# Performance work log

Measured on AMD Instinct MI355X. Metric: run time of the kernel, lower is better.

The kernel has to match this reference:

```python
import jax, jax.numpy as jnp
import numpy as np
import math

K = 2
CAPACITY = -1
NEED_L_AUX = True


def topk_gating(logits, k=K, capacity=CAPACITY, need_l_aux=NEED_L_AUX):
    # logits: (T, P, E) tokens x prototypes x experts-per-prototype
    gates = jax.nn.softmax(logits.astype(jnp.float32), axis=-1).astype(logits.dtype)
    T, P, E = gates.shape
    cap = int(math.ceil(1.25 * T / E)) if capacity < 0 else capacity

    idx1 = jnp.argmax(gates, axis=-1)                      # (T, P)
    mask1 = jax.nn.one_hot(idx1, E, dtype=jnp.int32)       # (T, P, E)
    loc1 = jnp.cumsum(mask1, axis=0) - 1                   # position in expert queue
    if need_l_aux:
        me = jnp.mean(gates, axis=0)
        ce = jnp.mean(mask1.astype(jnp.float32), axis=0)
        l_aux = jnp.mean(me * ce)
    else:
        l_aux = jnp.zeros((), jnp.float32)
    mask1 = mask1 * (loc1 < cap)                           # drop over-capacity tokens
    loc1_s = jnp.sum(loc1 * mask1, axis=-1)                # (T, P)
    gates1_s = jnp.sum(gates * mask1, axis=-1)
    denom = gates1_s
    gates_s_list = [gates1_s]
    mask_list = [mask1]
    loc_s_list = [loc1_s]
    last_logits = logits
    last_mask = mask1
    prev_masks = mask1
    for _ in range(2, k + 1):
        last_logits = jnp.where(last_mask.astype(bool), -jnp.inf, last_logits)
        idx = jnp.argmax(last_logits, axis=-1)
        mask = jax.nn.one_hot(idx, E, dtype=jnp.int32)
        loc = jnp.cumsum(mask, axis=0) - 1 + jnp.sum(prev_masks, axis=0, keepdims=True)
        mask = mask * (loc < cap)
        last_mask = mask
        prev_masks = prev_masks + mask
        mask_list.append(mask)
        loc_s_list.append(jnp.sum(loc * mask, axis=-1))
        gs = jnp.sum(gates * mask, axis=-1)
        denom = denom + gs
        gates_s_list.append(gs)
    denom = jnp.maximum(denom, jnp.finfo(denom.dtype).eps)

    combine = jnp.zeros((T, P, E, cap), gates.dtype)
    for gs, mask, ls in zip(gates_s_list, mask_list, loc_s_list):
        g = (gs / denom)[..., None] * mask                  # (T, P, E)
        loc_sc = jax.nn.one_hot(ls, cap, dtype=gates.dtype)  # (T, P, cap)
        combine = combine + g[..., None] * loc_sc[:, :, None, :]
    dispatch_mask = combine.astype(bool)
    return l_aux.astype(logits.dtype), combine.astype(logits.dtype), dispatch_mask


def setup_inputs() -> dict:
    key = jax.random.key(0)
    k1, k2 = jax.random.split(key)
    inp = jax.random.normal(k1, (4096, 2048), dtype=jnp.float32)
    W = jax.random.normal(k2, (64, 2048), dtype=jnp.float32) / math.sqrt(2048.0)
    return {"input": inp, "W": W, "bs": 4096, "prototypes": 2}


def reference(input, W, bs, prototypes):
    logits = input @ W.T                                   # (T, num_experts_total)
    logits = logits.reshape(input.shape[0], prototypes, -1)  # (T, P, E)
    return topk_gating(logits, k=K, capacity=CAPACITY, need_l_aux=NEED_L_AUX)
```

## Files before the change

kernel.cpp:

```cpp
#include <hip/hip_runtime.h>
#include <cstdint>

#define T_TOK 4096
#define KDIM 2048
#define NE 64
#define NP 2
#define EE 32
#define CAP 160
#define NKC 8
#define KCHUNK 256
#define BLKR 128
#define COMB_ELEMS 41943040ull
#define OUT_ELEMS 83886081ull
#define SMALLF 65536
#define NFB 4096
#define TOT4 20971520

__global__ __launch_bounds__(256) void k_fused(const float* __restrict__ x,
                                               const float* __restrict__ W,
                                               float* __restrict__ part,
                                               float* __restrict__ out,
                                               int s1lo, int s1hi, int s2lo, int s2hi,
                                               int fillLast) {
  __shared__ float xs[BLKR][36];
  __shared__ float wt[32][68];
  const int tid = threadIdx.x;
  if (blockIdx.x >= 256) {
    const int fb = blockIdx.x - 256;
    float4* p4 = reinterpret_cast<float4*>(out);
    const float4 z4 = make_float4(0.f, 0.f, 0.f, 0.f);
    const int start = fb * 5120;
#pragma unroll
    for (int j = 0; j < 20; ++j) {
      const int i4 = start + tid + j * 256;
      if (i4 >= s1lo && i4 < s1hi) continue;
      if (i4 >= s2lo && i4 < s2hi) continue;
      p4[i4] = z4;
    }
    if (fillLast && fb == NFB - 1 && tid == 255) out[OUT_ELEMS - 1] = 0.f;
    return;
  }
  const int rb = blockIdx.x & 31;
  const int kc = blockIdx.x >> 5;
  const int r0 = rb * BLKR;
  const int er = tid & 15;
  const int rg = tid >> 4;
  float acc[8][4];
#pragma unroll
  for (int i = 0; i < 8; ++i)
#pragma unroll
    for (int c = 0; c < 4; ++c) acc[i][c] = 0.f;

  float4 sx[4], sw[2];
  {
    const int kb = kc * KCHUNK;
#pragma unroll
    for (int q = 0; q < 4; ++q) {
      const int li = tid + q * 256, row = li >> 3, kq = (li & 7) * 4;
      sx[q] = *reinterpret_cast<const float4*>(&x[(size_t)(r0 + row) * KDIM + kb + kq]);
    }
#pragma unroll
    for (int q = 0; q < 2; ++q) {
      const int li = tid + q * 256, e = li >> 3, kq = (li & 7) * 4;
      sw[q] = *reinterpret_cast<const float4*>(&W[(size_t)e * KDIM + kb + kq]);
    }
  }
  for (int s = 0; s < 8; ++s) {
    __syncthreads();
#pragma unroll
    for (int q = 0; q < 4; ++q) {
      const int li = tid + q * 256, row = li >> 3, kq = (li & 7) * 4;
      *reinterpret_cast<float4*>(&xs[row][kq]) = sx[q];
    }
#pragma unroll
    for (int q = 0; q < 2; ++q) {
      const int li = tid + q * 256, e = li >> 3, kq = (li & 7) * 4;
      wt[kq][e] = sw[q].x; wt[kq + 1][e] = sw[q].y;
      wt[kq + 2][e] = sw[q].z; wt[kq + 3][e] = sw[q].w;
    }
    if (s < 7) {
      const int kb = kc * KCHUNK + (s + 1) * 32;
#pragma unroll
      for (int q = 0; q < 4; ++q) {
        const int li = tid + q * 256, row = li >> 3, kq = (li & 7) * 4;
        sx[q] = *reinterpret_cast<const float4*>(&x[(size_t)(r0 + row) * KDIM + kb + kq]);
      }
#pragma unroll
      for (int q = 0; q < 2; ++q) {
        const int li = tid + q * 256, e = li >> 3, kq = (li & 7) * 4;
        sw[q] = *reinterpret_cast<const float4*>(&W[(size_t)e * KDIM + kb + kq]);
      }
    }
    __syncthreads();
#pragma unroll
    for (int k4 = 0; k4 < 8; ++k4) {
      float4 wb[4];
#pragma unroll
      for (int j = 0; j < 4; ++j)
        wb[j] = *reinterpret_cast<const float4*>(&wt[k4 * 4 + j][er * 4]);
#pragma unroll
      for (int i = 0; i < 8; ++i) {
        const float4 xv = *reinterpret_cast<const float4*>(&xs[rg + 16 * i][k4 * 4]);
        acc[i][0] = fmaf(xv.w, wb[3].x, fmaf(xv.z, wb[2].x, fmaf(xv.y, wb[1].x, fmaf(xv.x, wb[0].x, acc[i][0]))));
        acc[i][1] = fmaf(xv.w, wb[3].y, fmaf(xv.z, wb[2].y, fmaf(xv.y, wb[1].y, fmaf(xv.x, wb[0].y, acc[i][1]))));
        acc[i][2] = fmaf(xv.w, wb[3].z, fmaf(xv.z, wb[2].z, fmaf(xv.y, wb[1].z, fmaf(xv.x, wb[0].z, acc[i][2]))));
        acc[i][3] = fmaf(xv.w, wb[3].w, fmaf(xv.z, wb[2].w, fmaf(xv.y, wb[1].w, fmaf(xv.x, wb[0].w, acc[i][3]))));
      }
    }
  }
#pragma unroll
  for (int i = 0; i < 8; ++i) {
    float4 v; v.x = acc[i][0]; v.y = acc[i][1]; v.z = acc[i][2]; v.w = acc[i][3];
    *reinterpret_cast<float4*>(
        &part[((size_t)kc * T_TOK + r0 + rg + 16 * i) * NE + er * 4]) = v;
  }
}

__global__ __launch_bounds__(256) void k_fill2(float* __restrict__ out) {
  float4* p4 = reinterpret_cast<float4*>(out + 4);
  const float4 z4 = make_float4(0.f, 0.f, 0.f, 0.f);
  const int base = blockIdx.x * 2048 + threadIdx.x;
#pragma unroll
  for (int j = 0; j < 8; ++j) p4[base + j * 256] = z4;
}

__global__ __launch_bounds__(64) void k_soft(const float* __restrict__ part,
                                             float2* __restrict__ g12,
                                             int* __restrict__ idxs,
                                             float* __restrict__ me_part) {
  __shared__ float lg[64][33];
  const int tid = threadIdx.x;
  const int R = blockIdx.x * 64 + tid;
  const int t = R >> 1;
  const int p = R & 1;
  float v[32];
  const float* pr = part + (size_t)t * NE + p * EE;
#pragma unroll
  for (int e = 0; e < 32; e += 4) {
    float4 s = *reinterpret_cast<const float4*>(pr + e);
    v[e] = s.x; v[e + 1] = s.y; v[e + 2] = s.z; v[e + 3] = s.w;
  }
  for (int kc = 1; kc < NKC; ++kc) {
    const float* prk = pr + (size_t)kc * T_TOK * NE;
#pragma unroll
    for (int e = 0; e < 32; e += 4) {
      float4 s = *reinterpret_cast<const float4*>(prk + e);
      v[e] += s.x; v[e + 1] += s.y; v[e + 2] += s.z; v[e + 3] += s.w;
    }
  }
  float m = v[0];
#pragma unroll
  for (int e = 1; e < 32; ++e) m = fmaxf(m, v[e]);
  float sum = 0.f;
#pragma unroll
  for (int e = 0; e < 32; ++e) { v[e] = expf(v[e] - m); sum += v[e]; }
  const float inv = 1.0f / sum;
#pragma unroll
  for (int e = 0; e < 32; ++e) v[e] *= inv;
  float g1 = -1.f; int i1 = 0;
#pragma unroll
  for (int e = 0; e < 32; ++e) if (v[e] > g1) { g1 = v[e]; i1 = e; }
  float g2 = -1.f; int i2 = 0;
#pragma unroll
  for (int e = 0; e < 32; ++e) if (e != i1 && v[e] > g2) { g2 = v[e]; i2 = e; }
  g12[R] = make_float2(g1, g2);
  idxs[R] = i1 | (i2 << 8);
#pragma unroll
  for (int e = 0; e < 32; ++e) lg[tid][e] = v[e];
  __syncthreads();
  {
    const int pp = tid >> 5, ee = tid & 31;
    float s = 0.f;
    for (int rr = pp; rr < 64; rr += 2) s += lg[rr][ee];
    me_part[blockIdx.x * 64 + tid] = s;
  }
}

__global__ __launch_bounds__(1024) void k_scan(const int* __restrict__ idxs,
                                               const float2* __restrict__ g12,
                                               const float* __restrict__ me_part,
                                               int2* __restrict__ fl,
                                               float2* __restrict__ wvp,
                                               float* __restrict__ out) {
  __shared__ int grp[NP][64][32];
  __shared__ int tot[NP][32];
  __shared__ unsigned short tk1[NP][T_TOK];
  __shared__ unsigned short tk2[NP][T_TOK];
  __shared__ float red[64];
  const int tid = threadIdx.x;
  const int wvi = tid >> 6;
  const int p = wvi >> 3;
  const int wg = wvi & 7;
  const int l = tid & 63;
  const unsigned long long lmask = (1ull << l) - 1ull;
  for (int gi = 0; gi < 8; ++gi) {
    const int g = wg * 8 + gi;
    const int t = g * 64 + l;
    const int e1 = idxs[t * 2 + p] & 255;
    if (l < 32) grp[p][g][l] = 0;
    unsigned long long m = ~0ull;
#pragma unroll
    for (int b = 0; b < 5; ++b) {
      const unsigned long long bm = __ballot((e1 >> b) & 1);
      m &= ((e1 >> b) & 1) ? bm : ~bm;
    }
    const int rank = (int)__popcll(m & lmask);
    if (rank == 0) grp[p][g][e1] = (int)__popcll(m);
    tk1[p][t] = (unsigned short)(rank | (e1 << 6));
  }
  __syncthreads();
  if (tid < 64) {
    const int pp = tid >> 5, ee = tid & 31;
    int s = 0;
    for (int g = 0; g < 64; ++g) { int vv = grp[pp][g][ee]; grp[pp][g][ee] = s; s += vv; }
    tot[pp][ee] = s;
  }
  __syncthreads();
  for (int gi = 0; gi < 8; ++gi) {
    const int g = wg * 8 + gi;
    const int t = g * 64 + l;
    const int vv = tk1[p][t];
    tk1[p][t] = (unsigned short)(grp[p][g][vv >> 6] + (vv & 63));
  }
  if (tid < 64) {
    float s = 0.f;
    for (int b = 0; b < 128; ++b) s += me_part[b * 64 + tid];
    red[tid] = s * (float)tot[tid >> 5][tid & 31];
  }
  __syncthreads();
  if (tid == 0) {
    float s = 0.f;
    for (int i = 0; i < 64; ++i) s += red[i];
    out[0] = s / (64.0f * 4096.0f * 4096.0f);
  }
  for (int gi = 0; gi < 8; ++gi) {
    const int g = wg * 8 + gi;
    const int t = g * 64 + l;
    const int ii = idxs[t * 2 + p];
    const int e2 = (tk1[p][t] < CAP) ? (ii >> 8) : (ii & 255);
    if (l < 32) grp[p][g][l] = 0;
    unsigned long long m = ~0ull;
#pragma unroll
    for (int b = 0; b < 5; ++b) {
      const unsigned long long bm = __ballot((e2 >> b) & 1);
      m &= ((e2 >> b) & 1) ? bm : ~bm;
    }
    const int rank = (int)__popcll(m & lmask);
    if (rank == 0) grp[p][g][e2] = (int)__popcll(m);
    tk2[p][t] = (unsigned short)(rank | (e2 << 6));
  }
  __syncthreads();
  if (tid < 64) {
    const int pp = tid >> 5, ee = tid & 31;
    int s = min(tot[pp][ee], CAP);
    for (int g = 0; g < 64; ++g) { int vv = grp[pp][g][ee]; grp[pp][g][ee] = s; s += vv; }
  }
  __syncthreads();
  for (int gi = 0; gi < 8; ++gi) {
    const int g = wg * 8 + gi;
    const int t = g * 64 + l;
    const int R = t * 2 + p;
    const int ii = idxs[R];
    const int e1 = ii & 255;
    const int loc1v = tk1[p][t];
    const bool kept1 = loc1v < CAP;
    const int v2 = tk2[p][t];
    const int rank2 = v2 & 63, e2 = v2 >> 6;
    const int loc2 = grp[p][g][e2] + rank2;
    const bool kept2 = loc2 < CAP;
    const float2 gg = g12[R];
    const float gs1 = kept1 ? gg.x : 0.f;
    const float g2v = kept1 ? gg.y : gg.x;
    const float gs2 = kept2 ? g2v : 0.f;
    const float den = fmaxf(gs1 + gs2, 1.1920929e-07f);
    fl[R] = make_int2(kept1 ? e1 * CAP + loc1v : -1, kept2 ? e2 * CAP + loc2 : -1);
    wvp[R] = make_float2(gs1 / den, gs2 / den);
  }
}

__global__ __launch_bounds__(256) void k_fix(const int2* __restrict__ fl,
                                             const float2* __restrict__ wvp,
                                             float* __restrict__ out,
                                             int rlimit) {
  const int R = blockIdx.x * 256 + threadIdx.x;
  const int2 f = fl[R];
  const float2 w = wvp[R];
  float* oc = out + 1 + (size_t)R * 5120;
  if (f.x >= 0) oc[f.x] = w.x;
  if (f.y >= 0) oc[f.y] = w.y;
  if (R < rlimit) {
    float* od = out + 1 + COMB_ELEMS + (size_t)R * 5120;
    if (f.x >= 0) od[f.x] = 1.0f;
    if (f.y >= 0) od[f.y] = 1.0f;
  }
}

__global__ __launch_bounds__(1024) void k_write_tail(const int2* __restrict__ fl,
                                                     float* __restrict__ out,
                                                     int nfullB) {
  __shared__ int2 sfl[16];
  const int tid = threadIdx.x;
  const int rstart = nfullB * 2;
  const int nr = 8192 - rstart;
  if (tid < nr) sfl[tid] = fl[rstart + tid];
  __syncthreads();
  const size_t base = 1 + COMB_ELEMS + (size_t)rstart * 5120;
  const int cnt = nr * 5120;
  const int nx4 = (cnt - 4) >> 2;
  float4* p4 = (float4*)(out + base + 3);
  const float4 z4 = make_float4(0.f, 0.f, 0.f, 0.f);
  for (int idx = tid; idx < nx4; idx += 1024) p4[idx] = z4;
  if (tid < 3) out[base + tid] = 0.f;
  if (tid == 3) out[base + cnt - 1] = 0.f;
  __syncthreads();
  if (tid < 2 * nr) {
    const int rr = rstart + (tid >> 1);
    const int2 f = sfl[tid >> 1];
    const int pos = (tid & 1) ? f.y : f.x;
    if (pos >= 0) out[1 + COMB_ELEMS + (size_t)rr * 5120 + pos] = 1.0f;
  }
}

extern "C" void kernel_launch(void* const* d_in, const int* in_sizes, int n_in,
                              void* d_out, int out_size, void* d_ws, size_t ws_size,
                              hipStream_t stream) {
  const float* x = (const float*)d_in[0];
  const float* W = (const float*)d_in[1];
  float* out = (float*)d_out;

  const size_t PARTF = (size_t)NKC * T_TOK * NE;

  float* small;
  float* part;
  int s1lo = 0, s1hi = 0, s2lo = 0, s2hi = 0, fillLast = 1;
  bool needFill2 = false;
  int nfullB = 4096, rlimit = 8192;
  if (ws_size >= (SMALLF + PARTF) * sizeof(float)) {
    small = (float*)d_ws;
    part = small + SMALLF;
  } else if (ws_size >= SMALLF * sizeof(float)) {
    small = (float*)d_ws;
    part = out + 4;
    s1lo = 1; s1hi = 1 + (int)(PARTF / 4);
    needFill2 = true;
  } else {
    const size_t tb = (OUT_ELEMS - SMALLF) & ~(size_t)3;
    small = out + tb;
    part = out + 4;
    s1lo = 1; s1hi = 1 + (int)(PARTF / 4);
    s2lo = (int)(tb / 4); s2hi = TOT4;
    fillLast = 0;
    needFill2 = true;
    nfullB = (int)((tb - 1 - COMB_ELEMS) / 10240);
    rlimit = nfullB * 2;
  }
  float2* g12 = (float2*)small;
  int* idxs = (int*)(small + 16384);
  float* me_part = small + 24576;
  int2* fl = (int2*)(small + 32768);
  float2* wvp = (float2*)(small + 49152);

  hipLaunchKernelGGL(k_fused, dim3(256 + NFB), dim3(256), 0, stream,
                     x, W, part, out, s1lo, s1hi, s2lo, s2hi, fillLast);
  hipLaunchKernelGGL(k_soft, dim3(128), dim3(64), 0, stream, part, g12, idxs, me_part);
  if (needFill2)
    hipLaunchKernelGGL(k_fill2, dim3(256), dim3(256), 0, stream, out);
  hipLaunchKernelGGL(k_scan, dim3(1), dim3(1024), 0, stream, idxs, g12, me_part, fl, wvp, out);
  hipLaunchKernelGGL(k_fix, dim3(32), dim3(256), 0, stream, fl, wvp, out, rlimit);
  if (nfullB < 4096)
    hipLaunchKernelGGL(k_write_tail, dim3(1), dim3(1024), 0, stream, fl, out, nfullB);
}
```

Baseline: 104.0 us.

## Fuse softmax/top-2 into GEMM blocks, dropping split-K partials

```diff
diff --git a/kernel.cpp b/kernel.cpp
--- a/kernel.cpp
+++ b/kernel.cpp
@@ -7,89 +7,65 @@
 #define NP 2
 #define EE 32
 #define CAP 160
-#define NKC 8
-#define KCHUNK 256
-#define BLKR 128
 #define COMB_ELEMS 41943040ull
 #define OUT_ELEMS 83886081ull
 #define SMALLF 65536
 #define NFB 4096
+#define NGB 128
 #define TOT4 20971520
 
 __global__ __launch_bounds__(256) void k_fused(const float* __restrict__ x,
                                                const float* __restrict__ W,
-                                               float* __restrict__ part,
+                                               float2* __restrict__ g12,
+                                               int* __restrict__ idxs,
+                                               float* __restrict__ me_part,
                                                float* __restrict__ out,
-                                               int s1lo, int s1hi, int s2lo, int s2hi,
-                                               int fillLast) {
-  __shared__ float xs[BLKR][36];
+                                               int s2lo, int s2hi, int fillLast) {
+  __shared__ float xs[32][36];
   __shared__ float wt[32][68];
   const int tid = threadIdx.x;
-  if (blockIdx.x >= 256) {
-    const int fb = blockIdx.x - 256;
+  if (blockIdx.x >= NGB) {
+    const int fb = blockIdx.x - NGB;
     float4* p4 = reinterpret_cast<float4*>(out);
     const float4 z4 = make_float4(0.f, 0.f, 0.f, 0.f);
     const int start = fb * 5120;
 #pragma unroll
     for (int j = 0; j < 20; ++j) {
       const int i4 = start + tid + j * 256;
-      if (i4 >= s1lo && i4 < s1hi) continue;
       if (i4 >= s2lo && i4 < s2hi) continue;
       p4[i4] = z4;
     }
     if (fillLast && fb == NFB - 1 && tid == 255) out[OUT_ELEMS - 1] = 0.f;
     return;
   }
-  const int rb = blockIdx.x & 31;
-  const int kc = blockIdx.x >> 5;
-  const int r0 = rb * BLKR;
+  const int r0 = blockIdx.x * 32;
   const int er = tid & 15;
   const int rg = tid >> 4;
-  float acc[8][4];
-#pragma unroll
-  for (int i = 0; i < 8; ++i)
-#pragma unroll
-    for (int c = 0; c < 4; ++c) acc[i][c] = 0.f;
-
-  float4 sx[4], sw[2];
+  const int lrow = tid >> 3, lkq = (tid & 7) * 4;
+  float tot[2][4], chunk[2][4];
+#pragma unroll
+  for (int i = 0; i < 2; ++i)
+#pragma unroll
+    for (int c = 0; c < 4; ++c) chunk[i][c] = 0.f;
+
+  float4 sx, sw0, sw1;
   {
-    const int kb = kc * KCHUNK;
-#pragma unroll
-    for (int q = 0; q < 4; ++q) {
-      const int li = tid + q * 256, row = li >> 3, kq = (li & 7) * 4;
-      sx[q] = *reinterpret_cast<const float4*>(&x[(size_t)(r0 + row) * KDIM + kb + kq]);
-    }
-#pragma unroll
-    for (int q = 0; q < 2; ++q) {
-      const int li = tid + q * 256, e = li >> 3, kq = (li & 7) * 4;
-      sw[q] = *reinterpret_cast<const float4*>(&W[(size_t)e * KDIM + kb + kq]);
-    }
-  }
-  for (int s = 0; s < 8; ++s) {
+    sx = *reinterpret_cast<const float4*>(&x[(size_t)(r0 + lrow) * KDIM + lkq]);
+    sw0 = *reinterpret_cast<const float4*>(&W[(size_t)lrow * KDIM + lkq]);
+    sw1 = *reinterpret_cast<const float4*>(&W[(size_t)(lrow + 32) * KDIM + lkq]);
+  }
+  for (int it = 0; it < 64; ++it) {
     __syncthreads();
-#pragma unroll
-    for (int q = 0; q < 4; ++q) {
-      const int li = tid + q * 256, row = li >> 3, kq = (li & 7) * 4;
-      *reinterpret_cast<float4*>(&xs[row][kq]) = sx[q];
-    }
-#pragma unroll
-    for (int q = 0; q < 2; ++q) {
-      const int li = tid + q * 256, e = li >> 3, kq = (li & 7) * 4;
-      wt[kq][e] = sw[q].x; wt[kq + 1][e] = sw[q].y;
-      wt[kq + 2][e] = sw[q].z; wt[kq + 3][e] = sw[q].w;
-    }
-    if (s < 7) {
-      const int kb = kc * KCHUNK + (s + 1) * 32;
-#pragma unroll
-      for (int q = 0; q < 4; ++q) {
-        const int li = tid + q * 256, row = li >> 3, kq = (li & 7) * 4;
-        sx[q] = *reinterpret_cast<const float4*>(&x[(size_t)(r0 + row) * KDIM + kb + kq]);
-      }
-#pragma unroll
-      for (int q = 0; q < 2; ++q) {
-        const int li = tid + q * 256, e = li >> 3, kq = (li & 7) * 4;
-        sw[q] = *reinterpret_cast<const float4*>(&W[(size_t)e * KDIM + kb + kq]);
-      }
+    *reinterpret_cast<float4*>(&xs[lrow][lkq]) = sx;
+    wt[lkq][lrow] = sw0.x; wt[lkq + 1][lrow] = sw0.y;
+    wt[lkq + 2][lrow] = sw0.z; wt[lkq + 3][lrow] = sw0.w;
+    wt[lkq][lrow + 32] = sw1.x; wt[lkq + 1][lrow + 32] = sw1.y;
+    wt[lkq + 2][lrow + 32] = sw1.z; wt[lkq + 3][lrow + 32] = sw1.w;
+    if (it < 63) {
+      const int kb = (it + 1) * 32;
+      sx = *reinterpret_cast<const float4*>(&x[(size_t)(r0 + lrow) * KDIM + kb + lkq]);
+      sw0 = *reinterpret_cast<const float4*>(&W[(size_t)lrow * KDIM + kb + lkq]);
+      sw1 = *reinterpret_cast<const float4*>(&W[(size_t)(lrow + 32) * KDIM + kb + lkq]);
     }
     __syncthreads();
 #pragma unroll
@@ -99,79 +75,69 @@
       for (int j = 0; j < 4; ++j)
         wb[j] = *reinterpret_cast<const float4*>(&wt[k4 * 4 + j][er * 4]);
 #pragma unroll
-      for (int i = 0; i < 8; ++i) {
-        const float4 xv = *reinterpret_cast<const float4*>(&xs[rg + 16 * i][k4 * 4]);
-        acc[i][0] = fmaf(xv.w, wb[3].x, fmaf(xv.z, wb[2].x, fmaf(xv.y, wb[1].x, fmaf(xv.x, wb[0].x, acc[i][0]))));
-        acc[i][1] = fmaf(xv.w, wb[3].y, fmaf(xv.z, wb[2].y, fmaf(xv.y, wb[1].y, fmaf(xv.x, wb[0].y, acc[i][1]))));
-        acc[i][2] = fmaf(xv.w, wb[3].z, fmaf(xv.z, wb[2].z, fmaf(xv.y, wb[1].z, fmaf(xv.x, wb[0].z, acc[i][2]))));
-        acc[i][3] = fmaf(xv.w, wb[3].w, fmaf(xv.z, wb[2].w, fmaf(xv.y, wb[1].w, fmaf(xv.x, wb[0].w, acc[i][3]))));
+      for (int i = 0; i < 2; ++i) {
+        const float4 xv = *reinterpret_cast<const float4*>(&xs[rg * 2 + i][k4 * 4]);
+        chunk[i][0] = fmaf(xv.w, wb[3].x, fmaf(xv.z, wb[2].x, fmaf(xv.y, wb[1].x, fmaf(xv.x, wb[0].x, chunk[i][0]))));
+        chunk[i][1] = fmaf(xv.w, wb[3].y, fmaf(xv.z, wb[2].y, fmaf(xv.y, wb[1].y, fmaf(xv.x, wb[0].y, chunk[i][1]))));
+        chunk[i][2] = fmaf(xv.w, wb[3].z, fmaf(xv.z, wb[2].z, fmaf(xv.y, wb[1].z, fmaf(xv.x, wb[0].z, chunk[i][2]))));
+        chunk[i][3] = fmaf(xv.w, wb[3].w, fmaf(xv.z, wb[2].w, fmaf(xv.y, wb[1].w, fmaf(xv.x, wb[0].w, chunk[i][3]))));
       }
     }
-  }
-#pragma unroll
-  for (int i = 0; i < 8; ++i) {
-    float4 v; v.x = acc[i][0]; v.y = acc[i][1]; v.z = acc[i][2]; v.w = acc[i][3];
-    *reinterpret_cast<float4*>(
-        &part[((size_t)kc * T_TOK + r0 + rg + 16 * i) * NE + er * 4]) = v;
-  }
-}
-
-__global__ __launch_bounds__(256) void k_fill2(float* __restrict__ out) {
-  float4* p4 = reinterpret_cast<float4*>(out + 4);
-  const float4 z4 = make_float4(0.f, 0.f, 0.f, 0.f);
-  const int base = blockIdx.x * 2048 + threadIdx.x;
-#pragma unroll
-  for (int j = 0; j < 8; ++j) p4[base + j * 256] = z4;
-}
-
-__global__ __launch_bounds__(64) void k_soft(const float* __restrict__ part,
-                                             float2* __restrict__ g12,
-                                             int* __restrict__ idxs,
-                                             float* __restrict__ me_part) {
-  __shared__ float lg[64][33];
-  const int tid = threadIdx.x;
-  const int R = blockIdx.x * 64 + tid;
-  const int t = R >> 1;
-  const int p = R & 1;
-  float v[32];
-  const float* pr = part + (size_t)t * NE + p * EE;
-#pragma unroll
-  for (int e = 0; e < 32; e += 4) {
-    float4 s = *reinterpret_cast<const float4*>(pr + e);
-    v[e] = s.x; v[e + 1] = s.y; v[e + 2] = s.z; v[e + 3] = s.w;
-  }
-  for (int kc = 1; kc < NKC; ++kc) {
-    const float* prk = pr + (size_t)kc * T_TOK * NE;
+    if ((it & 7) == 7) {
+#pragma unroll
+      for (int i = 0; i < 2; ++i)
+#pragma unroll
+        for (int c = 0; c < 4; ++c) {
+          if (it == 7) tot[i][c] = chunk[i][c];
+          else tot[i][c] += chunk[i][c];
+          chunk[i][c] = 0.f;
+        }
+    }
+  }
+  __syncthreads();
+#pragma unroll
+  for (int i = 0; i < 2; ++i) {
+    float4 v; v.x = tot[i][0]; v.y = tot[i][1]; v.z = tot[i][2]; v.w = tot[i][3];
+    *reinterpret_cast<float4*>(&wt[rg * 2 + i][er * 4]) = v;
+  }
+  __syncthreads();
+  if (tid < 64) {
+    const int row = tid >> 1, p = tid & 1;
+    float v[32];
 #pragma unroll
     for (int e = 0; e < 32; e += 4) {
-      float4 s = *reinterpret_cast<const float4*>(prk + e);
-      v[e] += s.x; v[e + 1] += s.y; v[e + 2] += s.z; v[e + 3] += s.w;
-    }
-  }
-  float m = v[0];
-#pragma unroll
-  for (int e = 1; e < 32; ++e) m = fmaxf(m, v[e]);
-  float sum = 0.f;
-#pragma unroll
-  for (int e = 0; e < 32; ++e) { v[e] = expf(v[e] - m); sum += v[e]; }
-  const float inv = 1.0f / sum;
-#pragma unroll
-  for (int e = 0; e < 32; ++e) v[e] *= inv;
-  float g1 = -1.f; int i1 = 0;
-#pragma unroll
-  for (int e = 0; e < 32; ++e) if (v[e] > g1) { g1 = v[e]; i1 = e; }
-  float g2 = -1.f; int i2 = 0;
-#pragma unroll
-  for (int e = 0; e < 32; ++e) if (e != i1 && v[e] > g2) { g2 = v[e]; i2 = e; }
-  g12[R] = make_float2(g1, g2);
-  idxs[R] = i1 | (i2 << 8);
-#pragma unroll
-  for (int e = 0; e < 32; ++e) lg[tid][e] = v[e];
-  __syncthreads();
-  {
+      const float4 s = *reinterpret_cast<const float4*>(&wt[row][p * 32 + e]);
+      v[e] = s.x; v[e + 1] = s.y; v[e + 2] = s.z; v[e + 3] = s.w;
+    }
+    float m = v[0];
+#pragma unroll
+    for (int e = 1; e < 32; ++e) m = fmaxf(m, v[e]);
+    float sum = 0.f;
+#pragma unroll
+    for (int e = 0; e < 32; ++e) { v[e] = expf(v[e] - m); sum += v[e]; }
+    const float inv = 1.0f / sum;
+#pragma unroll
+    for (int e = 0; e < 32; ++e) v[e] *= inv;
+    float g1 = -1.f; int i1 = 0;
+#pragma unroll
+    for (int e = 0; e < 32; ++e) if (v[e] > g1) { g1 = v[e]; i1 = e; }
+    float g2 = -1.f; int i2 = 0;
+#pragma unroll
+    for (int e = 0; e < 32; ++e) if (e != i1 && v[e] > g2) { g2 = v[e]; i2 = e; }
+    const int R = blockIdx.x * 64 + tid;
+    g12[R] = make_float2(g1, g2);
+    idxs[R] = i1 | (i2 << 8);
+#pragma unroll
+    for (int e = 0; e < 32; e += 4) {
+      float4 s; s.x = v[e]; s.y = v[e + 1]; s.z = v[e + 2]; s.w = v[e + 3];
+      *reinterpret_cast<float4*>(&wt[row][p * 32 + e]) = s;
+    }
+  }
+  __syncthreads();
+  if (tid < 64) {
     const int pp = tid >> 5, ee = tid & 31;
     float s = 0.f;
-    for (int rr = pp; rr < 64; rr += 2) s += lg[rr][ee];
+    for (int tok = 0; tok < 32; ++tok) s += wt[tok][pp * 32 + ee];
     me_part[blockIdx.x * 64 + tid] = s;
   }
 }
@@ -328,29 +294,16 @@
   const float* W = (const float*)d_in[1];
   float* out = (float*)d_out;
 
-  const size_t PARTF = (size_t)NKC * T_TOK * NE;
-
   float* small;
-  float* part;
-  int s1lo = 0, s1hi = 0, s2lo = 0, s2hi = 0, fillLast = 1;
-  bool needFill2 = false;
+  int s2lo = 0, s2hi = 0, fillLast = 1;
   int nfullB = 4096, rlimit = 8192;
-  if (ws_size >= (SMALLF + PARTF) * sizeof(float)) {
+  if (ws_size >= SMALLF * sizeof(float)) {
     small = (float*)d_ws;
-    part = small + SMALLF;
-  } else if (ws_size >= SMALLF * sizeof(float)) {
-    small = (float*)d_ws;
-    part = out + 4;
-    s1lo = 1; s1hi = 1 + (int)(PARTF / 4);
-    needFill2 = true;
   } else {
     const size_t tb = (OUT_ELEMS - SMALLF) & ~(size_t)3;
     small = out + tb;
-    part = out + 4;
-    s1lo = 1; s1hi = 1 + (int)(PARTF / 4);
     s2lo = (int)(tb / 4); s2hi = TOT4;
     fillLast = 0;
-    needFill2 = true;
     nfullB = (int)((tb - 1 - COMB_ELEMS) / 10240);
     rlimit = nfullB * 2;
   }
@@ -360,11 +313,8 @@
   int2* fl = (int2*)(small + 32768);
   float2* wvp = (float2*)(small + 49152);
 
-  hipLaunchKernelGGL(k_fused, dim3(256 + NFB), dim3(256), 0, stream,
-                     x, W, part, out, s1lo, s1hi, s2lo, s2hi, fillLast);
-  hipLaunchKernelGGL(k_soft, dim3(128), dim3(64), 0, stream, part, g12, idxs, me_part);
-  if (needFill2)
-    hipLaunchKernelGGL(k_fill2, dim3(256), dim3(256), 0, stream, out);
+  hipLaunchKernelGGL(k_fused, dim3(NGB + NFB), dim3(256), 0, stream,
+                     x, W, g12, idxs, me_part, out, s2lo, s2hi, fillLast);
   hipLaunchKernelGGL(k_scan, dim3(1), dim3(1024), 0, stream, idxs, g12, me_part, fl, wvp, out);
   hipLaunchKernelGGL(k_fix, dim3(32), dim3(256), 0, stream, fl, wvp, out, rlimit);
   if (nfullB < 4096)
```

New measurement: 125.9 us. +21.1%, slower.

## Fuse GEMM, softmax and output zero-fill into one cooperative persistent kernel

Applied to the files above, without the earlier changes.

```diff
diff --git a/kernel.cpp b/kernel.cpp
--- a/kernel.cpp
+++ b/kernel.cpp
@@ -1,5 +1,8 @@
 #include <hip/hip_runtime.h>
+#include <hip/hip_cooperative_groups.h>
 #include <cstdint>
+
+namespace cg = cooperative_groups;
 
 #define T_TOK 4096
 #define KDIM 2048
@@ -12,74 +15,61 @@
 #define BLKR 128
 #define COMB_ELEMS 41943040ull
 #define OUT_ELEMS 83886081ull
-#define SMALLF 65536
+#define SMALLF 65544
+#define PARTF 2097152ull
+#define TOT4 20971520
 #define NFB 4096
-#define TOT4 20971520
-
-__global__ __launch_bounds__(256) void k_fused(const float* __restrict__ x,
-                                               const float* __restrict__ W,
-                                               float* __restrict__ part,
-                                               float* __restrict__ out,
-                                               int s1lo, int s1hi, int s2lo, int s2hi,
-                                               int fillLast) {
-  __shared__ float xs[BLKR][36];
-  __shared__ float wt[32][68];
+#define UNITS 16384u
+#define RESERVE_B 1024u
+#define PB_F 81788928
+
+__device__ __forceinline__ void fill_units(float* __restrict__ out,
+                                           unsigned int* __restrict__ ctr,
+                                           unsigned int ubase, unsigned int uend,
+                                           int lane, int s1lo, int s1hi) {
+  float4* p4 = reinterpret_cast<float4*>(out);
+  const float4 z4 = make_float4(0.f, 0.f, 0.f, 0.f);
+  while (true) {
+    unsigned int u = 0;
+    if (lane == 0) u = atomicAdd(ctr, 1u);
+    u = (unsigned int)__builtin_amdgcn_readfirstlane((int)u) + ubase;
+    if (u >= uend) break;
+    const int b4 = (int)u * 1280 + lane;
+#pragma unroll
+    for (int j = 0; j < 20; ++j) {
+      const int i4 = b4 + j * 64;
+      if (i4 >= s1lo && i4 < s1hi) continue;
+      p4[i4] = z4;
+    }
+  }
+}
+
+__global__ __launch_bounds__(256)
+void k_coop(const float* __restrict__ x, const float* __restrict__ W,
+            float* __restrict__ part, float2* __restrict__ g12,
+            int* __restrict__ idxs, float* __restrict__ me_part,
+            float* __restrict__ out, unsigned int* __restrict__ ctr,
+            int s1lo, int s1hi) {
+  __shared__ union {
+    struct { float xs[BLKR][36]; float wt[32][68]; } g;
+    float lg[64][33];
+  } sh;
   const int tid = threadIdx.x;
-  if (blockIdx.x >= 256) {
-    const int fb = blockIdx.x - 256;
-    float4* p4 = reinterpret_cast<float4*>(out);
-    const float4 z4 = make_float4(0.f, 0.f, 0.f, 0.f);
-    const int start = fb * 5120;
-#pragma unroll
-    for (int j = 0; j < 20; ++j) {
-      const int i4 = start + tid + j * 256;
-      if (i4 >= s1lo && i4 < s1hi) continue;
-      if (i4 >= s2lo && i4 < s2hi) continue;
-      p4[i4] = z4;
-    }
-    if (fillLast && fb == NFB - 1 && tid == 255) out[OUT_ELEMS - 1] = 0.f;
-    return;
-  }
-  const int rb = blockIdx.x & 31;
-  const int kc = blockIdx.x >> 5;
-  const int r0 = rb * BLKR;
-  const int er = tid & 15;
-  const int rg = tid >> 4;
-  float acc[8][4];
-#pragma unroll
-  for (int i = 0; i < 8; ++i)
-#pragma unroll
-    for (int c = 0; c < 4; ++c) acc[i][c] = 0.f;
-
-  float4 sx[4], sw[2];
-  {
-    const int kb = kc * KCHUNK;
-#pragma unroll
-    for (int q = 0; q < 4; ++q) {
-      const int li = tid + q * 256, row = li >> 3, kq = (li & 7) * 4;
-      sx[q] = *reinterpret_cast<const float4*>(&x[(size_t)(r0 + row) * KDIM + kb + kq]);
-    }
-#pragma unroll
-    for (int q = 0; q < 2; ++q) {
-      const int li = tid + q * 256, e = li >> 3, kq = (li & 7) * 4;
-      sw[q] = *reinterpret_cast<const float4*>(&W[(size_t)e * KDIM + kb + kq]);
-    }
-  }
-  for (int s = 0; s < 8; ++s) {
-    __syncthreads();
-#pragma unroll
-    for (int q = 0; q < 4; ++q) {
-      const int li = tid + q * 256, row = li >> 3, kq = (li & 7) * 4;
-      *reinterpret_cast<float4*>(&xs[row][kq]) = sx[q];
-    }
-#pragma unroll
-    for (int q = 0; q < 2; ++q) {
-      const int li = tid + q * 256, e = li >> 3, kq = (li & 7) * 4;
-      wt[kq][e] = sw[q].x; wt[kq + 1][e] = sw[q].y;
-      wt[kq + 2][e] = sw[q].z; wt[kq + 3][e] = sw[q].w;
-    }
-    if (s < 7) {
-      const int kb = kc * KCHUNK + (s + 1) * 32;
+  const int lane = tid & 63;
+  if (blockIdx.x < 256) {
+    const int rb = (int)blockIdx.x & 31;
+    const int kc = (int)blockIdx.x >> 5;
+    const int r0 = rb * BLKR;
+    const int er = tid & 15;
+    const int rg = tid >> 4;
+    float acc[8][4];
+#pragma unroll
+    for (int i = 0; i < 8; ++i)
+#pragma unroll
+      for (int c = 0; c < 4; ++c) acc[i][c] = 0.f;
+    float4 sx[4], sw[2];
+    {
+      const int kb = kc * KCHUNK;
 #pragma unroll
       for (int q = 0; q < 4; ++q) {
         const int li = tid + q * 256, row = li >> 3, kq = (li & 7) * 4;
@@ -91,89 +81,109 @@
         sw[q] = *reinterpret_cast<const float4*>(&W[(size_t)e * KDIM + kb + kq]);
       }
     }
+    for (int s = 0; s < 8; ++s) {
+      __syncthreads();
+#pragma unroll
+      for (int q = 0; q < 4; ++q) {
+        const int li = tid + q * 256, row = li >> 3, kq = (li & 7) * 4;
+        *reinterpret_cast<float4*>(&sh.g.xs[row][kq]) = sx[q];
+      }
+#pragma unroll
+      for (int q = 0; q < 2; ++q) {
+        const int li = tid + q * 256, e = li >> 3, kq = (li & 7) * 4;
+        sh.g.wt[kq][e] = sw[q].x; sh.g.wt[kq + 1][e] = sw[q].y;
+        sh.g.wt[kq + 2][e] = sw[q].z; sh.g.wt[kq + 3][e] = sw[q].w;
+      }
+      if (s < 7) {
+        const int kb = kc * KCHUNK + (s + 1) * 32;
+#pragma unroll
+        for (int q = 0; q < 4; ++q) {
+          const int li = tid + q * 256, row = li >> 3, kq = (li & 7) * 4;
+          sx[q] = *reinterpret_cast<const float4*>(&x[(size_t)(r0 + row) * KDIM + kb + kq]);
+        }
+#pragma unroll
+        for (int q = 0; q < 2; ++q) {
+          const int li = tid + q * 256, e = li >> 3, kq = (li & 7) * 4;
+          sw[q] = *reinterpret_cast<const float4*>(&W[(size_t)e * KDIM + kb + kq]);
+        }
+      }
+      __syncthreads();
+#pragma unroll
+      for (int k4 = 0; k4 < 8; ++k4) {
+        float4 wb[4];
+#pragma unroll
+        for (int j = 0; j < 4; ++j)
+          wb[j] = *reinterpret_cast<const float4*>(&sh.g.wt[k4 * 4 + j][er * 4]);
+#pragma unroll
+        for (int i = 0; i < 8; ++i) {
+          const float4 xv = *reinterpret_cast<const float4*>(&sh.g.xs[rg + 16 * i][k4 * 4]);
+          acc[i][0] = fmaf(xv.w, wb[3].x, fmaf(xv.z, wb[2].x, fmaf(xv.y, wb[1].x, fmaf(xv.x, wb[0].x, acc[i][0]))));
+          acc[i][1] = fmaf(xv.w, wb[3].y, fmaf(xv.z, wb[2].y, fmaf(xv.y, wb[1].y, fmaf(xv.x, wb[0].y, acc[i][1]))));
+          acc[i][2] = fmaf(xv.w, wb[3].z, fmaf(xv.z, wb[2].z, fmaf(xv.y, wb[1].z, fmaf(xv.x, wb[0].z, acc[i][2]))));
+          acc[i][3] = fmaf(xv.w, wb[3].w, fmaf(xv.z, wb[2].w, fmaf(xv.y, wb[1].w, fmaf(xv.x, wb[0].w, acc[i][3]))));
+        }
+      }
+    }
+#pragma unroll
+    for (int i = 0; i < 8; ++i) {
+      float4 v; v.x = acc[i][0]; v.y = acc[i][1]; v.z = acc[i][2]; v.w = acc[i][3];
+      *reinterpret_cast<float4*>(
+          &part[((size_t)kc * T_TOK + r0 + rg + 16 * i) * NE + er * 4]) = v;
+    }
+  }
+  fill_units(out, ctr, 0u, UNITS - RESERVE_B, lane, s1lo, s1hi);
+  __threadfence();
+  cg::this_grid().sync();
+  if (blockIdx.x < 128) {
+    const int un = (int)blockIdx.x;
+    if (tid < 64) {
+      const int R = un * 64 + tid;
+      const int t = R >> 1, p = R & 1;
+      float v[32];
+      const float* pr = part + (size_t)t * NE + p * EE;
+#pragma unroll
+      for (int e = 0; e < 32; e += 4) {
+        const float4 s = *reinterpret_cast<const float4*>(pr + e);
+        v[e] = s.x; v[e + 1] = s.y; v[e + 2] = s.z; v[e + 3] = s.w;
+      }
+      for (int kc = 1; kc < NKC; ++kc) {
+        const float* prk = pr + (size_t)kc * T_TOK * NE;
+#pragma unroll
+        for (int e = 0; e < 32; e += 4) {
+          const float4 s = *reinterpret_cast<const float4*>(prk + e);
+          v[e] += s.x; v[e + 1] += s.y; v[e + 2] += s.z; v[e + 3] += s.w;
+        }
+      }
+      float m = v[0];
+#pragma unroll
+      for (int e = 1; e < 32; ++e) m = fmaxf(m, v[e]);
+      float sum = 0.f;
+#pragma unroll
+      for (int e = 0; e < 32; ++e) { v[e] = expf(v[e] - m); sum += v[e]; }
+      const float inv = 1.0f / sum;
+#pragma unroll
+      for (int e = 0; e < 32; ++e) v[e] *= inv;
+      float g1 = -1.f; int i1 = 0;
+#pragma unroll
+      for (int e = 0; e < 32; ++e) if (v[e] > g1) { g1 = v[e]; i1 = e; }
+      float g2 = -1.f; int i2 = 0;
+#pragma unroll
+      for (int e = 0; e < 32; ++e) if (e != i1 && v[e] > g2) { g2 = v[e]; i2 = e; }
+      g12[R] = make_float2(g1, g2);
+      idxs[R] = i1 | (i2 << 8);
+#pragma unroll
+      for (int e = 0; e < 32; ++e) sh.lg[tid][e] = v[e];
+    }
     __syncthreads();
-#pragma unroll
-    for (int k4 = 0; k4 < 8; ++k4) {
-      float4 wb[4];
-#pragma unroll
-      for (int j = 0; j < 4; ++j)
-        wb[j] = *reinterpret_cast<const float4*>(&wt[k4 * 4 + j][er * 4]);
-#pragma unroll
-      for (int i = 0; i < 8; ++i) {
-        const float4 xv = *reinterpret_cast<const float4*>(&xs[rg + 16 * i][k4 * 4]);
-        acc[i][0] = fmaf(xv.w, wb[3].x, fmaf(xv.z, wb[2].x, fmaf(xv.y, wb[1].x, fmaf(xv.x, wb[0].x, acc[i][0]))));
-        acc[i][1] = fmaf(xv.w, wb[3].y, fmaf(xv.z, wb[2].y, fmaf(xv.y, wb[1].y, fmaf(xv.x, wb[0].y, acc[i][1]))));
-        acc[i][2] = fmaf(xv.w, wb[3].z, fmaf(xv.z, wb[2].z, fmaf(xv.y, wb[1].z, fmaf(xv.x, wb[0].z, acc[i][2]))));
-        acc[i][3] = fmaf(xv.w, wb[3].w, fmaf(xv.z, wb[2].w, fmaf(xv.y, wb[1].w, fmaf(xv.x, wb[0].w, acc[i][3]))));
-      }
-    }
-  }
-#pragma unroll
-  for (int i = 0; i < 8; ++i) {
-    float4 v; v.x = acc[i][0]; v.y = acc[i][1]; v.z = acc[i][2]; v.w = acc[i][3];
-    *reinterpret_cast<float4*>(
-        &part[((size_t)kc * T_TOK + r0 + rg + 16 * i) * NE + er * 4]) = v;
-  }
-}
-
-__global__ __launch_bounds__(256) void k_fill2(float* __restrict__ out) {
-  float4* p4 = reinterpret_cast<float4*>(out + 4);
-  const float4 z4 = make_float4(0.f, 0.f, 0.f, 0.f);
-  const int base = blockIdx.x * 2048 + threadIdx.x;
-#pragma unroll
-  for (int j = 0; j < 8; ++j) p4[base + j * 256] = z4;
-}
-
-__global__ __launch_bounds__(64) void k_soft(const float* __restrict__ part,
-                                             float2* __restrict__ g12,
-                                             int* __restrict__ idxs,
-                                             float* __restrict__ me_part) {
-  __shared__ float lg[64][33];
-  const int tid = threadIdx.x;
-  const int R = blockIdx.x * 64 + tid;
-  const int t = R >> 1;
-  const int p = R & 1;
-  float v[32];
-  const float* pr = part + (size_t)t * NE + p * EE;
-#pragma unroll
-  for (int e = 0; e < 32; e += 4) {
-    float4 s = *reinterpret_cast<const float4*>(pr + e);
-    v[e] = s.x; v[e + 1] = s.y; v[e + 2] = s.z; v[e + 3] = s.w;
-  }
-  for (int kc = 1; kc < NKC; ++kc) {
-    const float* prk = pr + (size_t)kc * T_TOK * NE;
-#pragma unroll
-    for (int e = 0; e < 32; e += 4) {
-      float4 s = *reinterpret_cast<const float4*>(prk + e);
-      v[e] += s.x; v[e + 1] += s.y; v[e + 2] += s.z; v[e + 3] += s.w;
-    }
-  }
-  float m = v[0];
-#pragma unroll
-  for (int e = 1; e < 32; ++e) m = fmaxf(m, v[e]);
-  float sum = 0.f;
-#pragma unroll
-  for (int e = 0; e < 32; ++e) { v[e] = expf(v[e] - m); sum += v[e]; }
-  const float inv = 1.0f / sum;
-#pragma unroll
-  for (int e = 0; e < 32; ++e) v[e] *= inv;
-  float g1 = -1.f; int i1 = 0;
-#pragma unroll
-  for (int e = 0; e < 32; ++e) if (v[e] > g1) { g1 = v[e]; i1 = e; }
-  float g2 = -1.f; int i2 = 0;
-#pragma unroll
-  for (int e = 0; e < 32; ++e) if (e != i1 && v[e] > g2) { g2 = v[e]; i2 = e; }
-  g12[R] = make_float2(g1, g2);
-  idxs[R] = i1 | (i2 << 8);
-#pragma unroll
-  for (int e = 0; e < 32; ++e) lg[tid][e] = v[e];
-  __syncthreads();
-  {
-    const int pp = tid >> 5, ee = tid & 31;
-    float s = 0.f;
-    for (int rr = pp; rr < 64; rr += 2) s += lg[rr][ee];
-    me_part[blockIdx.x * 64 + tid] = s;
-  }
+    if (tid < 64) {
+      const int pp = tid >> 5, ee = tid & 31;
+      float s = 0.f;
+      for (int rr = pp; rr < 64; rr += 2) s += sh.lg[rr][ee];
+      me_part[un * 64 + tid] = s;
+    }
+    __syncthreads();
+  }
+  fill_units(out, ctr + 1, UNITS - RESERVE_B, UNITS, lane, s1lo, s1hi);
 }
 
 __global__ __launch_bounds__(1024) void k_scan(const int* __restrict__ idxs,
@@ -278,10 +288,191 @@
   }
 }
 
-__global__ __launch_bounds__(256) void k_fix(const int2* __restrict__ fl,
-                                             const float2* __restrict__ wvp,
-                                             float* __restrict__ out,
-                                             int rlimit) {
+__global__ __launch_bounds__(256) void k_fix2(const int2* __restrict__ fl,
+                                              const float2* __restrict__ wvp,
+                                              float* __restrict__ out) {
+  const int R = blockIdx.x * 256 + threadIdx.x;
+  const int2 f = fl[R];
+  const float2 w = wvp[R];
+  float* oc = out + 1 + (size_t)R * 5120;
+  float* od = out + 1 + COMB_ELEMS + (size_t)R * 5120;
+  if (R == 8191) od[5119] = 0.f;
+  if (f.x >= 0) { oc[f.x] = w.x; od[f.x] = 1.0f; }
+  if (f.y >= 0) { oc[f.y] = w.y; od[f.y] = 1.0f; }
+}
+
+__global__ __launch_bounds__(256) void k_tailB(float* __restrict__ out) {
+  float4* p4 = reinterpret_cast<float4*>(out);
+  const float4 z4 = make_float4(0.f, 0.f, 0.f, 0.f);
+  const int base = 20447232 + (int)blockIdx.x * 4096 + (int)threadIdx.x;
+#pragma unroll
+  for (int j = 0; j < 16; ++j) p4[base + j * 256] = z4;
+  if (blockIdx.x == 0 && threadIdx.x == 0) out[OUT_ELEMS - 1] = 0.f;
+}
+
+__global__ __launch_bounds__(256) void k_fusedF(const float* __restrict__ x,
+                                                const float* __restrict__ W,
+                                                float* __restrict__ part,
+                                                float* __restrict__ out,
+                                                int s1lo, int s1hi, int s2lo, int s2hi,
+                                                int fillLast) {
+  __shared__ float xs[BLKR][36];
+  __shared__ float wt[32][68];
+  const int tid = threadIdx.x;
+  if (blockIdx.x >= 256) {
+    const int fb = blockIdx.x - 256;
+    float4* p4 = reinterpret_cast<float4*>(out);
+    const float4 z4 = make_float4(0.f, 0.f, 0.f, 0.f);
+    const int start = fb * 5120;
+#pragma unroll
+    for (int j = 0; j < 20; ++j) {
+      const int i4 = start + tid + j * 256;
+      if (i4 >= s1lo && i4 < s1hi) continue;
+      if (i4 >= s2lo && i4 < s2hi) continue;
+      p4[i4] = z4;
+    }
+    if (fillLast && fb == NFB - 1 && tid == 255) out[OUT_ELEMS - 1] = 0.f;
+    return;
+  }
+  const int rb = blockIdx.x & 31;
+  const int kc = blockIdx.x >> 5;
+  const int r0 = rb * BLKR;
+  const int er = tid & 15;
+  const int rg = tid >> 4;
+  float acc[8][4];
+#pragma unroll
+  for (int i = 0; i < 8; ++i)
+#pragma unroll
+    for (int c = 0; c < 4; ++c) acc[i][c] = 0.f;
+  float4 sx[4], sw[2];
+  {
+    const int kb = kc * KCHUNK;
+#pragma unroll
+    for (int q = 0; q < 4; ++q) {
+      const int li = tid + q * 256, row = li >> 3, kq = (li & 7) * 4;
+      sx[q] = *reinterpret_cast<const float4*>(&x[(size_t)(r0 + row) * KDIM + kb + kq]);
+    }
+#pragma unroll
+    for (int q = 0; q < 2; ++q) {
+      const int li = tid + q * 256, e = li >> 3, kq = (li & 7) * 4;
+      sw[q] = *reinterpret_cast<const float4*>(&W[(size_t)e * KDIM + kb + kq]);
+    }
+  }
+  for (int s = 0; s < 8; ++s) {
+    __syncthreads();
+#pragma unroll
+    for (int q = 0; q < 4; ++q) {
+      const int li = tid + q * 256, row = li >> 3, kq = (li & 7) * 4;
+      *reinterpret_cast<float4*>(&xs[row][kq]) = sx[q];
+    }
+#pragma unroll
+    for (int q = 0; q < 2; ++q) {
+      const int li = tid + q * 256, e = li >> 3, kq = (li & 7) * 4;
+      wt[kq][e] = sw[q].x; wt[kq + 1][e] = sw[q].y;
+      wt[kq + 2][e] = sw[q].z; wt[kq + 3][e] = sw[q].w;
+    }
+    if (s < 7) {
+      const int kb = kc * KCHUNK + (s + 1) * 32;
+#pragma unroll
+      for (int q = 0; q < 4; ++q) {
+        const int li = tid + q * 256, row = li >> 3, kq = (li & 7) * 4;
+        sx[q] = *reinterpret_cast<const float4*>(&x[(size_t)(r0 + row) * KDIM + kb + kq]);
+      }
+#pragma unroll
+      for (int q = 0; q < 2; ++q) {
+        const int li = tid + q * 256, e = li >> 3, kq = (li & 7) * 4;
+        sw[q] = *reinterpret_cast<const float4*>(&W[(size_t)e * KDIM + kb + kq]);
+      }
+    }
+    __syncthreads();
+#pragma unroll
+    for (int k4 = 0; k4 < 8; ++k4) {
+      float4 wb[4];
+#pragma unroll
+      for (int j = 0; j < 4; ++j)
+        wb[j] = *reinterpret_cast<const float4*>(&wt[k4 * 4 + j][er * 4]);
+#pragma unroll
+      for (int i = 0; i < 8; ++i) {
+        const float4 xv = *reinterpret_cast<const float4*>(&xs[rg + 16 * i][k4 * 4]);
+        acc[i][0] = fmaf(xv.w, wb[3].x, fmaf(xv.z, wb[2].x, fmaf(xv.y, wb[1].x, fmaf(xv.x, wb[0].x, acc[i][0]))));
+        acc[i][1] = fmaf(xv.w, wb[3].y, fmaf(xv.z, wb[2].y, fmaf(xv.y, wb[1].y, fmaf(xv.x, wb[0].y, acc[i][1]))));
+        acc[i][2] = fmaf(xv.w, wb[3].z, fmaf(xv.z, wb[2].z, fmaf(xv.y, wb[1].z, fmaf(xv.x, wb[0].z, acc[i][2]))));
+        acc[i][3] = fmaf(xv.w, wb[3].w, fmaf(xv.z, wb[2].w, fmaf(xv.y, wb[1].w, fmaf(xv.x, wb[0].w, acc[i][3]))));
+      }
+    }
+  }
+#pragma unroll
+  for (int i = 0; i < 8; ++i) {
+    float4 v; v.x = acc[i][0]; v.y = acc[i][1]; v.z = acc[i][2]; v.w = acc[i][3];
+    *reinterpret_cast<float4*>(
+        &part[((size_t)kc * T_TOK + r0 + rg + 16 * i) * NE + er * 4]) = v;
+  }
+}
+
+__global__ __launch_bounds__(256) void k_fill2F(float* __restrict__ out) {
+  float4* p4 = reinterpret_cast<float4*>(out + 4);
+  const float4 z4 = make_float4(0.f, 0.f, 0.f, 0.f);
+  const int base = blockIdx.x * 2048 + threadIdx.x;
+#pragma unroll
+  for (int j = 0; j < 8; ++j) p4[base + j * 256] = z4;
+}
+
+__global__ __launch_bounds__(64) void k_softF(const float* __restrict__ part,
+                                              float2* __restrict__ g12,
+                                              int* __restrict__ idxs,
+                                              float* __restrict__ me_part) {
+  __shared__ float lg[64][33];
+  const int tid = threadIdx.x;
+  const int R = blockIdx.x * 64 + tid;
+  const int t = R >> 1;
+  const int p = R & 1;
+  float v[32];
+  const float* pr = part + (size_t)t * NE + p * EE;
+#pragma unroll
+  for (int e = 0; e < 32; e += 4) {
+    float4 s = *reinterpret_cast<const float4*>(pr + e);
+    v[e] = s.x; v[e + 1] = s.y; v[e + 2] = s.z; v[e + 3] = s.w;
+  }
+  for (int kc = 1; kc < NKC; ++kc) {
+    const float* prk = pr + (size_t)kc * T_TOK * NE;
+#pragma unroll
+    for (int e = 0; e < 32; e += 4) {
+      float4 s = *reinterpret_cast<const float4*>(prk + e);
+      v[e] += s.x; v[e + 1] += s.y; v[e + 2] += s.z; v[e + 3] += s.w;
+    }
+  }
+  float m = v[0];
+#pragma unroll
+  for (int e = 1; e < 32; ++e) m = fmaxf(m, v[e]);
+  float sum = 0.f;
+#pragma unroll
+  for (int e = 0; e < 32; ++e) { v[e] = expf(v[e] - m); sum += v[e]; }
+  const float inv = 1.0f / sum;
+#pragma unroll
+  for (int e = 0; e < 32; ++e) v[e] *= inv;
+  float g1 = -1.f; int i1 = 0;
+#pragma unroll
+  for (int e = 0; e < 32; ++e) if (v[e] > g1) { g1 = v[e]; i1 = e; }
+  float g2 = -1.f; int i2 = 0;
+#pragma unroll
+  for (int e = 0; e < 32; ++e) if (e != i1 && v[e] > g2) { g2 = v[e]; i2 = e; }
+  g12[R] = make_float2(g1, g2);
+  idxs[R] = i1 | (i2 << 8);
+#pragma unroll
+  for (int e = 0; e < 32; ++e) lg[tid][e] = v[e];
+  __syncthreads();
+  {
+    const int pp = tid >> 5, ee = tid & 31;
+    float s = 0.f;
+    for (int rr = pp; rr < 64; rr += 2) s += lg[rr][ee];
+    me_part[blockIdx.x * 64 + tid] = s;
+  }
+}
+
+__global__ __launch_bounds__(256) void k_fixF(const int2* __restrict__ fl,
+                                              const float2* __restrict__ wvp,
+                                              float* __restrict__ out,
+                                              int rlimit) {
   const int R = blockIdx.x * 256 + threadIdx.x;
   const int2 f = fl[R];
   const float2 w = wvp[R];
@@ -295,9 +486,9 @@
   }
 }
 
-__global__ __launch_bounds__(1024) void k_write_tail(const int2* __restrict__ fl,
-                                                     float* __restrict__ out,
-                                                     int nfullB) {
+__global__ __launch_bounds__(1024) void k_tailF(const int2* __restrict__ fl,
+                                                float* __restrict__ out,
+                                                int nfullB) {
   __shared__ int2 sfl[16];
   const int tid = threadIdx.x;
   const int rstart = nfullB * 2;
@@ -321,15 +512,8 @@
   }
 }
 
-extern "C" void kernel_launch(void* const* d_in, const int* in_sizes, int n_in,
-                              void* d_out, int out_size, void* d_ws, size_t ws_size,
-                              hipStream_t stream) {
-  const float* x = (const float*)d_in[0];
-  const float* W = (const float*)d_in[1];
-  float* out = (float*)d_out;
-
-  const size_t PARTF = (size_t)NKC * T_TOK * NE;
-
+static void launch_fallback(const float* x, const float* W, float* out,
+                            void* d_ws, size_t ws_size, hipStream_t stream) {
   float* small;
   float* part;
   int s1lo = 0, s1hi = 0, s2lo = 0, s2hi = 0, fillLast = 1;
@@ -359,14 +543,53 @@
   float* me_part = small + 24576;
   int2* fl = (int2*)(small + 32768);
   float2* wvp = (float2*)(small + 49152);
-
-  hipLaunchKernelGGL(k_fused, dim3(256 + NFB), dim3(256), 0, stream,
+  hipLaunchKernelGGL(k_fusedF, dim3(256 + NFB), dim3(256), 0, stream,
                      x, W, part, out, s1lo, s1hi, s2lo, s2hi, fillLast);
-  hipLaunchKernelGGL(k_soft, dim3(128), dim3(64), 0, stream, part, g12, idxs, me_part);
+  hipLaunchKernelGGL(k_softF, dim3(128), dim3(64), 0, stream, part, g12, idxs, me_part);
   if (needFill2)
-    hipLaunchKernelGGL(k_fill2, dim3(256), dim3(256), 0, stream, out);
+    hipLaunchKernelGGL(k_fill2F, dim3(256), dim3(256), 0, stream, out);
   hipLaunchKernelGGL(k_scan, dim3(1), dim3(1024), 0, stream, idxs, g12, me_part, fl, wvp, out);
-  hipLaunchKernelGGL(k_fix, dim3(32), dim3(256), 0, stream, fl, wvp, out, rlimit);
+  hipLaunchKernelGGL(k_fixF, dim3(32), dim3(256), 0, stream, fl, wvp, out, rlimit);
   if (nfullB < 4096)
-    hipLaunchKernelGGL(k_write_tail, dim3(1), dim3(1024), 0, stream, fl, out, nfullB);
-}
+    hipLaunchKernelGGL(k_tailF, dim3(1), dim3(1024), 0, stream, fl, out, nfullB);
+}
+
+extern "C" void kernel_launch(void* const* d_in, const int* in_sizes, int n_in,
+                              void* d_out, int out_size, void* d_ws, size_t ws_size,
+                              hipStream_t stream) {
+  const float* x = (const float*)d_in[0];
+  const float* W = (const float*)d_in[1];
+  float* out = (float*)d_out;
+
+  const bool pathA = ws_size >= (SMALLF + PARTF) * sizeof(float);
+  const bool pathB = !pathA && ws_size >= SMALLF * sizeof(float);
+  if (!pathA && !pathB) { launch_fallback(x, W, out, d_ws, ws_size, stream); return; }
+
+  float* small = (float*)d_ws;
+  float* part = pathA ? (small + SMALLF) : (out + PB_F);
+  const int s1lo = pathA ? 0 : 20447232;
+  const int s1hi = pathA ? 0 : TOT4;
+  float2* g12 = (float2*)small;
+  int* idxs = (int*)(small + 16384);
+  float* me_part = small + 24576;
+  int2* fl = (int2*)(small + 32768);
+  float2* wvp = (float2*)(small + 49152);
+  unsigned int* ctr = (unsigned int*)(small + 65536);
+
+  hipMemsetAsync(ctr, 0, 8, stream);
+  int nb = 0;
+  hipError_t oe = hipOccupancyMaxActiveBlocksPerMultiprocessor(&nb, k_coop, 256, 0);
+  int G = (oe == hipSuccess && nb > 0) ? nb * 256 : 256;
+  if (G > 2048) G = 2048;
+  void* args[] = {(void*)&x, (void*)&W, (void*)&part, (void*)&g12, (void*)&idxs,
+                  (void*)&me_part, (void*)&out, (void*)&ctr,
+                  (void*)&s1lo, (void*)&s1hi};
+  hipError_t ce = hipLaunchCooperativeKernel((const void*)k_coop, dim3(G), dim3(256),
+                                             args, 0, stream);
+  if (ce != hipSuccess) { launch_fallback(x, W, out, d_ws, ws_size, stream); return; }
+
+  hipLaunchKernelGGL(k_scan, dim3(1), dim3(1024), 0, stream, idxs, g12, me_part, fl, wvp, out);
+  if (pathB)
+    hipLaunchKernelGGL(k_tailB, dim3(128), dim3(256), 0, stream, out);
+  hipLaunchKernelGGL(k_fix2, dim3(32), dim3(256), 0, stream, fl, wvp, out);
+}
```

After: 354.1 us. 3.4x slower.
